# Performance work log

Measured on AMD Instinct MI355X. Metric: run time of the kernel, lower is better.

## Reference

```python
import jax, jax.numpy as jnp
import numpy as np

D = 1024   # model dim (hard-coded in ClsNet)
H = 16     # num_heads
HD = D // H
FF = 2048  # torch TransformerEncoderLayer default dim_feedforward
B, LX, LY = 8, 512, 512
EPS = 1e-5
NEG = -1e9


def setup_inputs() -> dict:
    key = jax.random.key(0)
    ks = jax.random.split(key, 16)
    s = 0.02
    inp = {
        "x": jax.random.normal(ks[0], (B, LX, D), jnp.float32),
        "y": jax.random.normal(ks[1], (B, LY, D), jnp.float32),
        "cls": jax.random.normal(ks[2], (D,), jnp.float32) * s,
        "sep": jax.random.normal(ks[3], (D,), jnp.float32) * s,
        "px": jax.random.normal(ks[4], (D,), jnp.float32) * s,
        "py": jax.random.normal(ks[5], (D,), jnp.float32) * s,
        "Wqkv": jax.random.normal(ks[6], (3 * D, D), jnp.float32) * s,
        "bqkv": jnp.zeros((3 * D,), jnp.float32),
        "Wo": jax.random.normal(ks[7], (D, D), jnp.float32) * s,
        "bo": jnp.zeros((D,), jnp.float32),
        "W1": jax.random.normal(ks[8], (FF, D), jnp.float32) * s,
        "b1": jnp.zeros((FF,), jnp.float32),
        "W2": jax.random.normal(ks[9], (D, FF), jnp.float32) * s,
        "b2": jnp.zeros((D,), jnp.float32),
        "ln1_g": jnp.ones((D,), jnp.float32),
        "ln1_b": jnp.zeros((D,), jnp.float32),
        "ln2_g": jnp.ones((D,), jnp.float32),
        "ln2_b": jnp.zeros((D,), jnp.float32),
        "x_len": jax.random.randint(ks[10], (B,), 1, LX + 1, jnp.int32),
        "y_len": jax.random.randint(ks[11], (B,), 1, LY + 1, jnp.int32),
    }
    return inp


def _merge(x, y, cls, sep, px, py, x_len, y_len):
    # Vectorized version of ClsNet.merge: [CLS] x_i+px ... [SEP] y_i+py ... [SEP] pad...
    Bn, Lx, Dd = x.shape
    Ly = y.shape[1]
    S = Lx + Ly + 3
    pos = jnp.arange(S)[None, :]            # [1,S]
    lx = x_len[:, None]                     # [B,1]
    ly = y_len[:, None]
    is_cls = pos == 0                       # [1,S]
    is_x = (pos >= 1) & (pos <= lx)         # [B,S]
    is_sep1 = pos == lx + 1
    is_y = (pos >= lx + 2) & (pos <= lx + ly + 1)
    is_sep2 = pos == lx + ly + 2
    xi = jnp.clip(pos - 1, 0, Lx - 1)       # [1,S]
    yi = jnp.clip(pos - lx - 2, 0, Ly - 1)  # [B,S]
    xg = jnp.take_along_axis(x, xi[:, :, None], axis=1)  # [B,S,D] (broadcast batch)
    yg = jnp.take_along_axis(y, yi[:, :, None], axis=1)  # [B,S,D]
    seq = (jnp.where(is_x[..., None], xg + px, 0.0)
           + jnp.where(is_y[..., None], yg + py, 0.0)
           + is_cls[..., None] * cls
           + (is_sep1 | is_sep2)[..., None] * sep)       # [B,S,D]
    mask = is_cls | is_x | is_sep1 | is_y | is_sep2      # [B,S] True = valid token
    return seq, mask


def _ln(h, g, b):
    m = jnp.mean(h, axis=-1, keepdims=True)
    v = jnp.mean(jnp.square(h - m), axis=-1, keepdims=True)
    return (h - m) * jax.lax.rsqrt(v + EPS) * g + b


def _encoder_layer(seq, mask, Wqkv, bqkv, Wo, bo, W1, b1, W2, b2, ln1_g, ln1_b, ln2_g, ln2_b):
    Bn, S, Dd = seq.shape
    qkv = seq @ Wqkv.T + bqkv                              # [B,S,3D]
    q, k, v = jnp.split(qkv, 3, axis=-1)
    q = q.reshape(Bn, S, H, HD)
    k = k.reshape(Bn, S, H, HD)
    v = v.reshape(Bn, S, H, HD)
    bias = jnp.where(mask, 0.0, NEG)[:, None, None, :]     # padded KEYS masked out
    scores = jnp.einsum("bqhd,bkhd->bhqk", q, k) / np.sqrt(HD) + bias
    attn = jax.nn.softmax(scores, axis=-1)
    o = jnp.einsum("bhqk,bkhd->bqhd", attn, v).reshape(Bn, S, Dd)
    o = o @ Wo.T + bo
    h = _ln(seq + o, ln1_g, ln1_b)                          # post-norm (torch default)
    f = jax.nn.relu(h @ W1.T + b1) @ W2.T + b2
    return _ln(h + f, ln2_g, ln2_b)


def reference(x, y, cls, sep, px, py, Wqkv, bqkv, Wo, bo, W1, b1, W2, b2,
              ln1_g, ln1_b, ln2_g, ln2_b, x_len, y_len):
    seq, mask = _merge(x, y, cls, sep, px, py, x_len, y_len)
    out = _encoder_layer(seq, mask, Wqkv, bqkv, Wo, bo, W1, b1, W2, b2,
                         ln1_g, ln1_b, ln2_g, ln2_b)
    # torch code returns a[0] of the seq-first tensor -> the CLS position for all batches
    return out[:, 0, :]
```

## Files before the change

kernel.cpp:

```cpp
#include <hip/hip_runtime.h>
#include <hip/hip_bf16.h>

#define D_ 1024
#define H_ 16
#define FF_ 2048
#define B_ 8
#define S_ 1027
#define MPAD_ 8320
#define PSTR_ 1056
#define EPS_ 1e-5f

typedef __hip_bfloat16 bf16;
typedef unsigned short u16;
typedef unsigned int u32;
typedef __attribute__((ext_vector_type(4))) float floatx4;
typedef __bf16 bf16x8 __attribute__((ext_vector_type(8)));

__device__ __forceinline__ float2 bfpair(u32 u) {
  union { u32 u; float f; } lo, hi;
  lo.u = u << 16; hi.u = u & 0xffff0000u;
  return make_float2(lo.f, hi.f);
}

__device__ __forceinline__ u32 f2bfbits(float f) {
  union { bf16 h; u16 u; } cv; cv.h = __float2bfloat16(f); return (u32)cv.u;
}

__device__ __forceinline__ float block_sum(float x, float* red) {
  const int t = threadIdx.x;
  __syncthreads();
  red[t] = x;
  __syncthreads();
  for (int s = 128; s > 0; s >>= 1) {
    if (t < s) red[t] += red[t + s];
    __syncthreads();
  }
  return red[0];
}

__device__ __forceinline__ float block_max(float x, float* red) {
  const int t = threadIdx.x;
  __syncthreads();
  red[t] = x;
  __syncthreads();
  for (int s = 128; s > 0; s >>= 1) {
    if (t < s) red[t] = fmaxf(red[t], red[t + s]);
    __syncthreads();
  }
  return red[0];
}

__global__ void __launch_bounds__(256) build_seq_kernel(
    const float* __restrict__ x, const float* __restrict__ y,
    const float* __restrict__ cls, const float* __restrict__ sep,
    const float* __restrict__ px, const float* __restrict__ py,
    const int* __restrict__ x_len, const int* __restrict__ y_len,
    bf16* __restrict__ seq) {
  const int m = blockIdx.x, t = threadIdx.x;
  const int b = m / S_;
  const int s = m - b * S_;
  if (b >= B_) return;
  const float* src = nullptr;
  const float* add = nullptr;
  const int lx = x_len[b], ly = y_len[b];
  if (s == 0) src = cls;
  else if (s <= lx) { src = x + ((size_t)b * 512 + (s - 1)) * D_; add = px; }
  else if (s == lx + 1) src = sep;
  else if (s <= lx + ly + 1) { src = y + ((size_t)b * 512 + (s - lx - 2)) * D_; add = py; }
  else if (s == lx + ly + 2) src = sep;
  if (!src) return;
  float4 sv = ((const float4*)src)[t];
  if (add) {
    float4 av = ((const float4*)add)[t];
    sv.x += av.x; sv.y += av.y; sv.z += av.z; sv.w += av.w;
  }
  uint2 o;
  o.x = f2bfbits(sv.x) | (f2bfbits(sv.y) << 16);
  o.y = f2bfbits(sv.z) | (f2bfbits(sv.w) << 16);
  ((uint2*)(seq + (size_t)m * D_))[t] = o;
}

__global__ void __launch_bounds__(256) qr_kernel(
    const float* __restrict__ cls, const float* __restrict__ Wqkv,
    const float* __restrict__ bqkv, u16* __restrict__ RT_hi,
    u16* __restrict__ RT_lo) {
  const int cc = blockIdx.x, h = blockIdx.y, t = threadIdx.x;
  __shared__ float clds[D_];
  __shared__ float qs[64];
  *(float4*)&clds[t * 4] = ((const float4*)cls)[t];
  __syncthreads();
  const int w = t >> 6, l = t & 63;
#pragma unroll 2
  for (int e8 = 0; e8 < 16; ++e8) {
    const int e = e8 * 4 + w;
    const float4* wr = (const float4*)(Wqkv + (size_t)(h * 64 + e) * D_) + l;
    float acc = 0.f;
#pragma unroll
    for (int c = 0; c < 4; ++c) {
      float4 wv = wr[c * 64];
      const float* cp = &clds[c * 256 + l * 4];
      acc += wv.x * cp[0] + wv.y * cp[1] + wv.z * cp[2] + wv.w * cp[3];
    }
#pragma unroll
    for (int off = 32; off > 0; off >>= 1) acc += __shfl_down(acc, off, 64);
    if (l == 0) qs[e] = (acc + bqkv[h * 64 + e]) * 0.125f;
  }
  __syncthreads();
  const int c = cc * 256 + t;
  const float* Wk = Wqkv + (size_t)(D_ + h * 64) * D_ + c;
  float acc = 0.f;
#pragma unroll 8
  for (int e = 0; e < 64; ++e) acc += Wk[(size_t)e * D_] * qs[e];
  const u32 hb = f2bfbits(acc);
  union { u32 u; float f; } hv; hv.u = hb << 16;
  RT_hi[h * D_ + c] = (u16)hb;
  RT_lo[h * D_ + c] = (u16)f2bfbits(acc - hv.f);
}

__global__ void __launch_bounds__(256) scores_kernel(
    const bf16* __restrict__ seq, const u16* __restrict__ RT_hi,
    const u16* __restrict__ RT_lo, const int* __restrict__ x_len,
    const int* __restrict__ y_len, float* __restrict__ S) {
  const int m0 = blockIdx.x * 64;
  bool valid = false;
#pragma unroll
  for (int b = 0; b < B_; ++b) {
    int rs = b * S_, re = rs + x_len[b] + y_len[b] + 3;
    if (m0 < re && m0 + 64 > rs) valid = true;
  }
  if (!valid) return;
  const int t = threadIdx.x;
  const int w = t >> 6, lane = t & 63, lane16 = lane & 15, quad = lane >> 4;
  const int row = m0 + w * 16 + lane16;
  const u16* arow = (const u16*)seq + (size_t)row * D_ + quad * 8;
  const u16* bh = RT_hi + lane16 * D_ + quad * 8;
  const u16* bl = RT_lo + lane16 * D_ + quad * 8;
  floatx4 acc = {};
#pragma unroll
  for (int kt = 0; kt < 32; ++kt) {
    bf16x8 a  = *(const bf16x8*)(arow + kt * 32);
    bf16x8 vh = *(const bf16x8*)(bh + kt * 32);
    bf16x8 vl = *(const bf16x8*)(bl + kt * 32);
    acc = __builtin_amdgcn_mfma_f32_16x16x32_bf16(a, vh, acc, 0, 0, 0);
    acc = __builtin_amdgcn_mfma_f32_16x16x32_bf16(a, vl, acc, 0, 0, 0);
  }
  *(floatx4*)&S[(size_t)lane16 * MPAD_ + m0 + w * 16 + quad * 4] = acc;
}

__global__ void __launch_bounds__(256) softmax_kernel(
    const float* __restrict__ S, const int* __restrict__ x_len,
    const int* __restrict__ y_len, u16* __restrict__ P) {
  const int h = blockIdx.x, b = blockIdx.y, t = threadIdx.x;
  const int n = x_len[b] + y_len[b] + 3;
  __shared__ float sc[PSTR_];
  __shared__ float red[256];
  const float* Sp = S + (size_t)h * MPAD_ + b * S_;
  float lmax = -3.0e38f;
  for (int k = t; k < n; k += 256) {
    float s = Sp[k];
    sc[k] = s;
    lmax = fmaxf(lmax, s);
  }
  const float gmax = block_max(lmax, red);
  float lsum = 0.f;
  for (int k = t; k < n; k += 256) {
    float p = __expf(sc[k] - gmax);
    sc[k] = p;
    lsum += p;
  }
  const float inv = 1.0f / block_sum(lsum, red);
  u16* Pp = P + (size_t)(h * 8 + b) * PSTR_;
  for (int k = t; k < PSTR_; k += 256)
    Pp[k] = (k < n) ? (u16)f2bfbits(sc[k] * inv) : (u16)0;
}

__global__ void __launch_bounds__(256) cbar_kernel(
    const bf16* __restrict__ seq, const u16* __restrict__ P,
    const int* __restrict__ x_len, const int* __restrict__ y_len,
    float* __restrict__ cbar) {
  const int ct = blockIdx.x, b = blockIdx.y, t = threadIdx.x;
  const int c0 = ct * 64;
  const int n = x_len[b] + y_len[b] + 3;
  const int nkt = (n + 31) >> 5;
  __shared__ u16 tile[32 * 68];
  const int w = t >> 6, lane = t & 63, lane16 = lane & 15, quad = lane >> 4;
  const int sk = t >> 3, scg = (t & 7) * 8;
  floatx4 acc = {};
  for (int kt = 0; kt < nkt; ++kt) {
    const int k0 = kt * 32;
    __syncthreads();
    uint4 v = make_uint4(0u, 0u, 0u, 0u);
    if (k0 + sk < n)
      v = *(const uint4*)((const u16*)seq + (size_t)(b * S_ + k0 + sk) * D_ + c0 + scg);
    *(uint2*)&tile[sk * 68 + scg]     = make_uint2(v.x, v.y);
    *(uint2*)&tile[sk * 68 + scg + 4] = make_uint2(v.z, v.w);
    __syncthreads();
    bf16x8 a = *(const bf16x8*)(P + (size_t)(lane16 * 8 + b) * PSTR_ + k0 + quad * 8);
    union { bf16x8 v; u16 u[8]; } bu;
#pragma unroll
    for (int j = 0; j < 8; ++j)
      bu.u[j] = tile[(quad * 8 + j) * 68 + w * 16 + lane16];
    acc = __builtin_amdgcn_mfma_f32_16x16x32_bf16(a, bu.v, acc, 0, 0, 0);
  }
#pragma unroll
  for (int r = 0; r < 4; ++r)
    cbar[(size_t)(b * 16 + quad * 4 + r) * D_ + c0 + w * 16 + lane16] = acc[r];
}

template <int K, int N, int BSTR, bool INBF, bool OUTBF, bool RELU, bool PERHEAD>
__global__ void __launch_bounds__(256) gemv8_kernel(
    const void* __restrict__ in_, const float* __restrict__ W,
    const float* __restrict__ bias, void* __restrict__ out_) {
  const int t = threadIdx.x;
  const int hoff = PERHEAD ? ((blockIdx.x * 4) >> 6) * D_ : 0;
  __shared__ u16 lsb[INBF ? 8 * K : 1];
  __shared__ float lsf[INBF ? 1 : 8 * K];
  if (INBF) {
    const u16* in = (const u16*)in_;
    const int per = 8 * K / (256 * 8);
#pragma unroll
    for (int i = 0; i < per; ++i) {
      int flat = (t + i * 256) * 8;
      int b = flat / K, k = flat % K;
      *(uint4*)&lsb[flat] = *(const uint4*)(in + (size_t)b * BSTR + hoff + k);
    }
  } else {
    const float* in = (const float*)in_;
    const int per = 8 * K / (256 * 4);
#pragma unroll
    for (int i = 0; i < per; ++i) {
      int flat = (t + i * 256) * 4;
      int b = flat / K, k = flat % K;
      *(float4*)&lsf[flat] = *(const float4*)(in + (size_t)b * BSTR + hoff + k);
    }
  }
  __syncthreads();
  const int w = t >> 6, l = t & 63;
  const int r = blockIdx.x * 4 + w;
  float acc[8] = {};
#pragma unroll
  for (int ch = 0; ch < K / 256; ++ch) {
    float4 wv = *(const float4*)(W + (size_t)r * K + ch * 256 + l * 4);
#pragma unroll
    for (int b = 0; b < 8; ++b) {
      float i0, i1, i2, i3;
      if (INBF) {
        uint2 u = *(const uint2*)&lsb[b * K + ch * 256 + l * 4];
        float2 p0 = bfpair(u.x), p1 = bfpair(u.y);
        i0 = p0.x; i1 = p0.y; i2 = p1.x; i3 = p1.y;
      } else {
        const float* p = &lsf[b * K + ch * 256 + l * 4];
        i0 = p[0]; i1 = p[1]; i2 = p[2]; i3 = p[3];
      }
      acc[b] += wv.x * i0 + wv.y * i1 + wv.z * i2 + wv.w * i3;
    }
  }
#pragma unroll
  for (int off = 32; off > 0; off >>= 1)
#pragma unroll
    for (int b = 0; b < 8; ++b) acc[b] += __shfl_down(acc[b], off, 64);
  if (l == 0) {
    const float bs = bias[r];
#pragma unroll
    for (int b = 0; b < 8; ++b) {
      float v = acc[b] + bs;
      if (RELU) v = fmaxf(v, 0.f);
      if (OUTBF) ((bf16*)out_)[(size_t)b * N + r] = __float2bfloat16(v);
      else       ((float*)out_)[(size_t)b * N + r] = v;
    }
  }
}

__global__ void __launch_bounds__(256) w1ln_kernel(
    const float* __restrict__ att, const float* __restrict__ cls,
    const float* __restrict__ g1, const float* __restrict__ be1,
    const float* __restrict__ W1, const float* __restrict__ b1,
    bf16* __restrict__ f1) {
  const int t = threadIdx.x;
  __shared__ float ls[8 * D_];
  __shared__ float mn[8], rsd[8];
  float4 cv = ((const float4*)cls)[t];
#pragma unroll
  for (int i = 0; i < 8; ++i) {
    float4 a = ((const float4*)(att + (size_t)i * D_))[t];
    a.x += cv.x; a.y += cv.y; a.z += cv.z; a.w += cv.w;
    *(float4*)&ls[i * D_ + t * 4] = a;
  }
  __syncthreads();
  {
    const int b = t >> 5, j = t & 31;
    const float* base = &ls[b * D_ + j * 32];
    float s = 0.f, s2 = 0.f;
#pragma unroll
    for (int k = 0; k < 32; ++k) { float v = base[k]; s += v; s2 += v * v; }
#pragma unroll
    for (int off = 16; off > 0; off >>= 1) {
      s += __shfl_down(s, off, 32);
      s2 += __shfl_down(s2, off, 32);
    }
    if (j == 0) {
      float mean = s * (1.f / D_);
      mn[b] = mean;
      rsd[b] = rsqrtf(s2 * (1.f / D_) - mean * mean + EPS_);
    }
  }
  __syncthreads();
  {
    const int b = t >> 5, j = t & 31;
    const float mean = mn[b], rs = rsd[b];
    float* base = &ls[b * D_ + j * 32];
    const float* gp = &g1[j * 32];
    const float* bp = &be1[j * 32];
#pragma unroll
    for (int k = 0; k < 32; ++k)
      base[k] = (base[k] - mean) * rs * gp[k] + bp[k];
  }
  __syncthreads();
  const int w = t >> 6, l = t & 63;
  const int r = blockIdx.x * 4 + w;
  float acc[8] = {};
#pragma unroll
  for (int ch = 0; ch < 4; ++ch) {
    float4 wv = *(const float4*)(W1 + (size_t)r * D_ + ch * 256 + l * 4);
#pragma unroll
    for (int b = 0; b < 8; ++b) {
      const float* p = &ls[b * D_ + ch * 256 + l * 4];
      acc[b] += wv.x * p[0] + wv.y * p[1] + wv.z * p[2] + wv.w * p[3];
    }
  }
#pragma unroll
  for (int off = 32; off > 0; off >>= 1)
#pragma unroll
    for (int b = 0; b < 8; ++b) acc[b] += __shfl_down(acc[b], off, 64);
  if (l == 0) {
    const float bs = b1[r];
#pragma unroll
    for (int b = 0; b < 8; ++b)
      f1[(size_t)b * FF_ + r] = __float2bfloat16(fmaxf(acc[b] + bs, 0.f));
  }
}

__global__ void __launch_bounds__(256) ln2_kernel(
    const float* __restrict__ cls, const float* __restrict__ att,
    const float* __restrict__ f2, const float* __restrict__ g1,
    const float* __restrict__ be1, const float* __restrict__ g2,
    const float* __restrict__ be2, float* __restrict__ out) {
  const int b = blockIdx.x, t = threadIdx.x;
  __shared__ float v[D_];
  __shared__ float red[256];
  for (int i = t; i < D_; i += 256) v[i] = cls[i] + att[(size_t)b * D_ + i];
  __syncthreads();
  float ls = 0.f;
  for (int i = t; i < D_; i += 256) ls += v[i];
  const float m1 = block_sum(ls, red) * (1.f / D_);
  float lv = 0.f;
  for (int i = t; i < D_; i += 256) { float dk = v[i] - m1; lv += dk * dk; }
  const float rs1 = rsqrtf(block_sum(lv, red) * (1.f / D_) + EPS_);
  __syncthreads();
  for (int i = t; i < D_; i += 256)
    v[i] = (v[i] - m1) * rs1 * g1[i] + be1[i] + f2[(size_t)b * D_ + i];
  __syncthreads();
  float ls2 = 0.f;
  for (int i = t; i < D_; i += 256) ls2 += v[i];
  const float m2 = block_sum(ls2, red) * (1.f / D_);
  float lv2 = 0.f;
  for (int i = t; i < D_; i += 256) { float dk = v[i] - m2; lv2 += dk * dk; }
  const float rs2 = rsqrtf(block_sum(lv2, red) * (1.f / D_) + EPS_);
  for (int i = t; i < D_; i += 256)
    out[(size_t)b * D_ + i] = (v[i] - m2) * rs2 * g2[i] + be2[i];
}

extern "C" void kernel_launch(void* const* d_in, const int* in_sizes, int n_in,
                              void* d_out, int out_size, void* d_ws, size_t ws_size,
                              hipStream_t stream) {
  (void)in_sizes; (void)n_in; (void)out_size; (void)ws_size;
  const float* x    = (const float*)d_in[0];
  const float* y    = (const float*)d_in[1];
  const float* cls  = (const float*)d_in[2];
  const float* sep  = (const float*)d_in[3];
  const float* px   = (const float*)d_in[4];
  const float* py   = (const float*)d_in[5];
  const float* Wqkv = (const float*)d_in[6];
  const float* bqkv = (const float*)d_in[7];
  const float* Wo   = (const float*)d_in[8];
  const float* bo   = (const float*)d_in[9];
  const float* W1   = (const float*)d_in[10];
  const float* b1   = (const float*)d_in[11];
  const float* W2   = (const float*)d_in[12];
  const float* b2   = (const float*)d_in[13];
  const float* g1   = (const float*)d_in[14];
  const float* be1  = (const float*)d_in[15];
  const float* g2   = (const float*)d_in[16];
  const float* be2  = (const float*)d_in[17];
  const int* xl     = (const int*)d_in[18];
  const int* yl     = (const int*)d_in[19];

  char* ws = (char*)d_ws;
  bf16*  seq   = (bf16*)(ws);
  u16*   RT_hi = (u16*)(ws + 17039360);
  u16*   RT_lo = (u16*)(ws + 17072128);
  float* S     = (float*)(ws + 17104896);
  u16*   P     = (u16*)(ws + 17637376);
  float* cbar  = (float*)(ws + 17907712);
  float* o0    = (float*)(ws + 18432000);
  float* att   = (float*)(ws + 18464768);
  bf16*  f1    = (bf16*)(ws + 18497536);
  float* f2    = (float*)(ws + 18530304);

  build_seq_kernel<<<MPAD_, 256, 0, stream>>>(x, y, cls, sep, px, py, xl, yl, seq);
  qr_kernel<<<dim3(4, 16), 256, 0, stream>>>(cls, Wqkv, bqkv, RT_hi, RT_lo);
  scores_kernel<<<130, 256, 0, stream>>>(seq, RT_hi, RT_lo, xl, yl, S);
  softmax_kernel<<<dim3(16, 8), 256, 0, stream>>>(S, xl, yl, P);
  cbar_kernel<<<dim3(16, 8), 256, 0, stream>>>(seq, P, xl, yl, cbar);
  gemv8_kernel<1024, 1024, 16384, false, false, false, true>
      <<<256, 256, 0, stream>>>(cbar, Wqkv + (size_t)2048 * 1024, bqkv + 2048, o0);
  gemv8_kernel<1024, 1024, 1024, false, false, false, false>
      <<<256, 256, 0, stream>>>(o0, Wo, bo, att);
  w1ln_kernel<<<512, 256, 0, stream>>>(att, cls, g1, be1, W1, b1, f1);
  gemv8_kernel<2048, 1024, 2048, true, false, false, false>
      <<<256, 256, 0, stream>>>(f1, W2, b2, f2);
  ln2_kernel<<<B_, 256, 0, stream>>>(cls, att, f2, g1, be1, g2, be2,
                                     (float*)d_out);
}
```

Before: 205.9 us.

## Fuse all encoder stages into one cooperative persistent kernel with grid syncs

```diff
diff --git a/kernel.cpp b/kernel.cpp
--- a/kernel.cpp
+++ b/kernel.cpp
@@ -1,5 +1,8 @@
 #include <hip/hip_runtime.h>
 #include <hip/hip_bf16.h>
+#include <hip/hip_cooperative_groups.h>
+
+namespace cg = cooperative_groups;
 
 #define D_ 1024
 #define H_ 16
@@ -48,6 +51,359 @@
     __syncthreads();
   }
   return red[0];
+}
+
+struct SMemD { float sc[PSTR_]; float red[256]; };
+struct SMemJ { float v[D_]; float red[256]; };
+union SMemU {
+  float qs_[64];
+  SMemD d;
+  u16 tile[32 * 68];
+  float lsf[8 * D_];
+  u16 lsb[8 * FF_];
+  SMemJ j;
+};
+struct SMem { SMemU u; float mn[8]; float rsd[8]; };
+
+__global__ void __launch_bounds__(256) fused_kernel2(
+    const float* __restrict__ x, const float* __restrict__ y,
+    const float* __restrict__ cls, const float* __restrict__ sep,
+    const float* __restrict__ px, const float* __restrict__ py,
+    const float* __restrict__ Wqkv, const float* __restrict__ bqkv,
+    const float* __restrict__ Wo, const float* __restrict__ bo,
+    const float* __restrict__ W1, const float* __restrict__ b1,
+    const float* __restrict__ W2, const float* __restrict__ b2,
+    const float* __restrict__ g1, const float* __restrict__ be1,
+    const float* __restrict__ g2, const float* __restrict__ be2,
+    const int* __restrict__ xl, const int* __restrict__ yl,
+    bf16* __restrict__ seq, float* __restrict__ q0s,
+    u16* __restrict__ RT_hi, u16* __restrict__ RT_lo,
+    float* __restrict__ S, u16* __restrict__ P, float* __restrict__ cbar,
+    float* __restrict__ o0, float* __restrict__ att, bf16* __restrict__ f1,
+    float* __restrict__ f2, float* __restrict__ outv) {
+  cg::grid_group grid = cg::this_grid();
+  const int bid = blockIdx.x, t = threadIdx.x;
+  const int w = t >> 6, l = t & 63;
+  const int lane16 = l & 15, quad = l >> 4;
+  __shared__ SMem sm;
+
+  {
+    const int r = bid * 4 + w;
+    const float4* wr = (const float4*)(Wqkv + (size_t)r * D_) + l;
+    const float4* cl4 = (const float4*)cls + l;
+    float acc = 0.f;
+#pragma unroll
+    for (int c = 0; c < 4; ++c) {
+      float4 wv = wr[c * 64], cv = cl4[c * 64];
+      acc += wv.x * cv.x + wv.y * cv.y + wv.z * cv.z + wv.w * cv.w;
+    }
+#pragma unroll
+    for (int off = 32; off > 0; off >>= 1) acc += __shfl_down(acc, off, 64);
+    if (l == 0) q0s[r] = (acc + bqkv[r]) * 0.125f;
+  }
+  for (int m = bid; m < B_ * S_; m += 256) {
+    const int b = m / S_;
+    const int s = m - b * S_;
+    const float* src = nullptr;
+    const float* add = nullptr;
+    const int lx = xl[b], ly = yl[b];
+    if (s == 0) src = cls;
+    else if (s <= lx) { src = x + ((size_t)b * 512 + (s - 1)) * D_; add = px; }
+    else if (s == lx + 1) src = sep;
+    else if (s <= lx + ly + 1) { src = y + ((size_t)b * 512 + (s - lx - 2)) * D_; add = py; }
+    else if (s == lx + ly + 2) src = sep;
+    if (!src) continue;
+    float4 sv = ((const float4*)src)[t];
+    if (add) {
+      float4 av = ((const float4*)add)[t];
+      sv.x += av.x; sv.y += av.y; sv.z += av.z; sv.w += av.w;
+    }
+    uint2 o;
+    o.x = f2bfbits(sv.x) | (f2bfbits(sv.y) << 16);
+    o.y = f2bfbits(sv.z) | (f2bfbits(sv.w) << 16);
+    ((uint2*)(seq + (size_t)m * D_))[t] = o;
+  }
+  grid.sync();
+
+  if (bid < 64) {
+    const int h = bid >> 2, cc = bid & 3;
+    if (t < 64) sm.u.qs_[t] = q0s[h * 64 + t];
+    __syncthreads();
+    const int c = cc * 256 + t;
+    const float* Wk = Wqkv + (size_t)(D_ + h * 64) * D_ + c;
+    float acc = 0.f;
+#pragma unroll 8
+    for (int e = 0; e < 64; ++e) acc += Wk[(size_t)e * D_] * sm.u.qs_[e];
+    const u32 hb = f2bfbits(acc);
+    union { u32 u; float f; } hv; hv.u = hb << 16;
+    RT_hi[h * D_ + c] = (u16)hb;
+    RT_lo[h * D_ + c] = (u16)f2bfbits(acc - hv.f);
+  }
+  grid.sync();
+
+  if (bid < 130) {
+    const int m0 = bid * 64;
+    bool valid = false;
+#pragma unroll
+    for (int b = 0; b < B_; ++b) {
+      int rs = b * S_, re = rs + xl[b] + yl[b] + 3;
+      if (m0 < re && m0 + 64 > rs) valid = true;
+    }
+    if (valid) {
+      const int row = m0 + w * 16 + lane16;
+      const u16* arow = (const u16*)seq + (size_t)row * D_ + quad * 8;
+      const u16* bh = RT_hi + lane16 * D_ + quad * 8;
+      const u16* bl = RT_lo + lane16 * D_ + quad * 8;
+      floatx4 acc = {};
+#pragma unroll 4
+      for (int kt = 0; kt < 32; ++kt) {
+        bf16x8 a  = *(const bf16x8*)(arow + kt * 32);
+        bf16x8 vh = *(const bf16x8*)(bh + kt * 32);
+        bf16x8 vl = *(const bf16x8*)(bl + kt * 32);
+        acc = __builtin_amdgcn_mfma_f32_16x16x32_bf16(a, vh, acc, 0, 0, 0);
+        acc = __builtin_amdgcn_mfma_f32_16x16x32_bf16(a, vl, acc, 0, 0, 0);
+      }
+      *(floatx4*)&S[(size_t)lane16 * MPAD_ + m0 + w * 16 + quad * 4] = acc;
+    }
+  }
+  grid.sync();
+
+  if (bid < 128) {
+    const int h = bid >> 3, b = bid & 7;
+    const int n = xl[b] + yl[b] + 3;
+    const float* Sp = S + (size_t)h * MPAD_ + b * S_;
+    float lmax = -3.0e38f;
+    for (int k = t; k < n; k += 256) {
+      float s = Sp[k];
+      sm.u.d.sc[k] = s;
+      lmax = fmaxf(lmax, s);
+    }
+    const float gmax = block_max(lmax, sm.u.d.red);
+    float lsum = 0.f;
+    for (int k = t; k < n; k += 256) {
+      float p = __expf(sm.u.d.sc[k] - gmax);
+      sm.u.d.sc[k] = p;
+      lsum += p;
+    }
+    const float inv = 1.0f / block_sum(lsum, sm.u.d.red);
+    u16* Pp = P + (size_t)(h * 8 + b) * PSTR_;
+    for (int k = t; k < PSTR_; k += 256)
+      Pp[k] = (k < n) ? (u16)f2bfbits(sm.u.d.sc[k] * inv) : (u16)0;
+  }
+  grid.sync();
+
+  if (bid < 128) {
+    const int ct = bid >> 3, b = bid & 7;
+    const int c0 = ct * 64;
+    const int n = xl[b] + yl[b] + 3;
+    const int nkt = (n + 31) >> 5;
+    const int sk = t >> 3, scg = (t & 7) * 8;
+    const u16* Pp = P + (size_t)(lane16 * 8 + b) * PSTR_;
+    floatx4 acc = {};
+    for (int kt = 0; kt < nkt; ++kt) {
+      const int k0 = kt * 32;
+      __syncthreads();
+      uint4 v = make_uint4(0u, 0u, 0u, 0u);
+      if (k0 + sk < n)
+        v = *(const uint4*)((const u16*)seq + (size_t)(b * S_ + k0 + sk) * D_ + c0 + scg);
+      *(uint2*)&sm.u.tile[sk * 68 + scg]     = make_uint2(v.x, v.y);
+      *(uint2*)&sm.u.tile[sk * 68 + scg + 4] = make_uint2(v.z, v.w);
+      __syncthreads();
+      bf16x8 a = *(const bf16x8*)(Pp + k0 + quad * 8);
+      union { bf16x8 v; u16 u[8]; } bu;
+#pragma unroll
+      for (int j = 0; j < 8; ++j)
+        bu.u[j] = sm.u.tile[(quad * 8 + j) * 68 + w * 16 + lane16];
+      acc = __builtin_amdgcn_mfma_f32_16x16x32_bf16(a, bu.v, acc, 0, 0, 0);
+    }
+#pragma unroll
+    for (int r = 0; r < 4; ++r)
+      cbar[(size_t)(b * 16 + quad * 4 + r) * D_ + c0 + w * 16 + lane16] = acc[r];
+  }
+  grid.sync();
+
+  {
+    const int hoff = (bid >> 4) * D_;
+#pragma unroll
+    for (int i = 0; i < 8; ++i) {
+      int flat = (t + i * 256) * 4;
+      int b = flat >> 10, k = flat & 1023;
+      *(float4*)&sm.u.lsf[flat] = *(const float4*)(cbar + (size_t)b * 16384 + hoff + k);
+    }
+    __syncthreads();
+    const int r = bid * 4 + w;
+    const float* Wv = Wqkv + (size_t)2048 * D_;
+    float acc[8] = {};
+#pragma unroll
+    for (int ch = 0; ch < 4; ++ch) {
+      float4 wv = *(const float4*)(Wv + (size_t)r * D_ + ch * 256 + l * 4);
+#pragma unroll
+      for (int b = 0; b < 8; ++b) {
+        const float* p = &sm.u.lsf[b * D_ + ch * 256 + l * 4];
+        acc[b] += wv.x * p[0] + wv.y * p[1] + wv.z * p[2] + wv.w * p[3];
+      }
+    }
+#pragma unroll
+    for (int off = 32; off > 0; off >>= 1)
+#pragma unroll
+      for (int b = 0; b < 8; ++b) acc[b] += __shfl_down(acc[b], off, 64);
+    if (l == 0) {
+      const float bs = bqkv[2048 + r];
+#pragma unroll
+      for (int b = 0; b < 8; ++b) o0[(size_t)b * D_ + r] = acc[b] + bs;
+    }
+  }
+  grid.sync();
+
+  {
+#pragma unroll
+    for (int i = 0; i < 8; ++i) {
+      int flat = (t + i * 256) * 4;
+      *(float4*)&sm.u.lsf[flat] = *(const float4*)(o0 + flat);
+    }
+    __syncthreads();
+    const int r = bid * 4 + w;
+    float acc[8] = {};
+#pragma unroll
+    for (int ch = 0; ch < 4; ++ch) {
+      float4 wv = *(const float4*)(Wo + (size_t)r * D_ + ch * 256 + l * 4);
+#pragma unroll
+      for (int b = 0; b < 8; ++b) {
+        const float* p = &sm.u.lsf[b * D_ + ch * 256 + l * 4];
+        acc[b] += wv.x * p[0] + wv.y * p[1] + wv.z * p[2] + wv.w * p[3];
+      }
+    }
+#pragma unroll
+    for (int off = 32; off > 0; off >>= 1)
+#pragma unroll
+      for (int b = 0; b < 8; ++b) acc[b] += __shfl_down(acc[b], off, 64);
+    if (l == 0) {
+      const float bs = bo[r];
+#pragma unroll
+      for (int b = 0; b < 8; ++b) att[(size_t)b * D_ + r] = acc[b] + bs;
+    }
+  }
+  grid.sync();
+
+  {
+    float4 cv = ((const float4*)cls)[t];
+#pragma unroll
+    for (int i = 0; i < 8; ++i) {
+      float4 a = ((const float4*)(att + (size_t)i * D_))[t];
+      a.x += cv.x; a.y += cv.y; a.z += cv.z; a.w += cv.w;
+      *(float4*)&sm.u.lsf[i * D_ + t * 4] = a;
+    }
+    __syncthreads();
+    {
+      const int b = t >> 5, j = t & 31;
+      const float* base = &sm.u.lsf[b * D_ + j * 32];
+      float s = 0.f, s2 = 0.f;
+#pragma unroll
+      for (int k = 0; k < 32; ++k) { float v = base[k]; s += v; s2 += v * v; }
+#pragma unroll
+      for (int off = 16; off > 0; off >>= 1) {
+        s += __shfl_down(s, off, 32);
+        s2 += __shfl_down(s2, off, 32);
+      }
+      if (j == 0) {
+        float mean = s * (1.f / D_);
+        sm.mn[b] = mean;
+        sm.rsd[b] = rsqrtf(s2 * (1.f / D_) - mean * mean + EPS_);
+      }
+    }
+    __syncthreads();
+    {
+      const int b = t >> 5, j = t & 31;
+      const float mean = sm.mn[b], rs = sm.rsd[b];
+      float* base = &sm.u.lsf[b * D_ + j * 32];
+      const float* gp = &g1[j * 32];
+      const float* bp = &be1[j * 32];
+#pragma unroll
+      for (int k = 0; k < 32; ++k)
+        base[k] = (base[k] - mean) * rs * gp[k] + bp[k];
+    }
+    __syncthreads();
+#pragma unroll
+    for (int rr = 0; rr < 2; ++rr) {
+      const int r = bid * 8 + rr * 4 + w;
+      float acc[8] = {};
+#pragma unroll
+      for (int ch = 0; ch < 4; ++ch) {
+        float4 wv = *(const float4*)(W1 + (size_t)r * D_ + ch * 256 + l * 4);
+#pragma unroll
+        for (int b = 0; b < 8; ++b) {
+          const float* p = &sm.u.lsf[b * D_ + ch * 256 + l * 4];
+          acc[b] += wv.x * p[0] + wv.y * p[1] + wv.z * p[2] + wv.w * p[3];
+        }
+      }
+#pragma unroll
+      for (int off = 32; off > 0; off >>= 1)
+#pragma unroll
+        for (int b = 0; b < 8; ++b) acc[b] += __shfl_down(acc[b], off, 64);
+      if (l == 0) {
+        const float bs = b1[r];
+#pragma unroll
+        for (int b = 0; b < 8; ++b)
+          f1[(size_t)b * FF_ + r] = __float2bfloat16(fmaxf(acc[b] + bs, 0.f));
+      }
+    }
+  }
+  grid.sync();
+
+  {
+#pragma unroll
+    for (int i = 0; i < 8; ++i) {
+      int flat = (t + i * 256) * 8;
+      *(uint4*)&sm.u.lsb[flat] = *(const uint4*)((const u16*)f1 + flat);
+    }
+    __syncthreads();
+    const int r = bid * 4 + w;
+    float acc[8] = {};
+#pragma unroll
+    for (int ch = 0; ch < 8; ++ch) {
+      float4 wv = *(const float4*)(W2 + (size_t)r * FF_ + ch * 256 + l * 4);
+#pragma unroll
+      for (int b = 0; b < 8; ++b) {
+        uint2 u = *(const uint2*)&sm.u.lsb[b * FF_ + ch * 256 + l * 4];
+        float2 p0 = bfpair(u.x), p1 = bfpair(u.y);
+        acc[b] += wv.x * p0.x + wv.y * p0.y + wv.z * p1.x + wv.w * p1.y;
+      }
+    }
+#pragma unroll
+    for (int off = 32; off > 0; off >>= 1)
+#pragma unroll
+      for (int b = 0; b < 8; ++b) acc[b] += __shfl_down(acc[b], off, 64);
+    if (l == 0) {
+      const float bs = b2[r];
+#pragma unroll
+      for (int b = 0; b < 8; ++b) f2[(size_t)b * D_ + r] = acc[b] + bs;
+    }
+  }
+  grid.sync();
+
+  if (bid < 8) {
+    const int b = bid;
+    for (int i = t; i < D_; i += 256) sm.u.j.v[i] = cls[i] + att[(size_t)b * D_ + i];
+    __syncthreads();
+    float ls = 0.f;
+    for (int i = t; i < D_; i += 256) ls += sm.u.j.v[i];
+    const float m1 = block_sum(ls, sm.u.j.red) * (1.f / D_);
+    float lv = 0.f;
+    for (int i = t; i < D_; i += 256) { float dk = sm.u.j.v[i] - m1; lv += dk * dk; }
+    const float rs1 = rsqrtf(block_sum(lv, sm.u.j.red) * (1.f / D_) + EPS_);
+    __syncthreads();
+    for (int i = t; i < D_; i += 256)
+      sm.u.j.v[i] = (sm.u.j.v[i] - m1) * rs1 * g1[i] + be1[i] + f2[(size_t)b * D_ + i];
+    __syncthreads();
+    float ls2 = 0.f;
+    for (int i = t; i < D_; i += 256) ls2 += sm.u.j.v[i];
+    const float m2 = block_sum(ls2, sm.u.j.red) * (1.f / D_);
+    float lv2 = 0.f;
+    for (int i = t; i < D_; i += 256) { float dk = sm.u.j.v[i] - m2; lv2 += dk * dk; }
+    const float rs2 = rsqrtf(block_sum(lv2, sm.u.j.red) * (1.f / D_) + EPS_);
+    for (int i = t; i < D_; i += 256)
+      outv[(size_t)b * D_ + i] = (sm.u.j.v[i] - m2) * rs2 * g2[i] + be2[i];
+  }
 }
 
 __global__ void __launch_bounds__(256) build_seq_kernel(
@@ -136,7 +492,7 @@
   const u16* bh = RT_hi + lane16 * D_ + quad * 8;
   const u16* bl = RT_lo + lane16 * D_ + quad * 8;
   floatx4 acc = {};
-#pragma unroll
+#pragma unroll 4
   for (int kt = 0; kt < 32; ++kt) {
     bf16x8 a  = *(const bf16x8*)(arow + kt * 32);
     bf16x8 vh = *(const bf16x8*)(bh + kt * 32);
@@ -397,28 +753,41 @@
 
   char* ws = (char*)d_ws;
   bf16*  seq   = (bf16*)(ws);
-  u16*   RT_hi = (u16*)(ws + 17039360);
-  u16*   RT_lo = (u16*)(ws + 17072128);
-  float* S     = (float*)(ws + 17104896);
-  u16*   P     = (u16*)(ws + 17637376);
-  float* cbar  = (float*)(ws + 17907712);
-  float* o0    = (float*)(ws + 18432000);
-  float* att   = (float*)(ws + 18464768);
-  bf16*  f1    = (bf16*)(ws + 18497536);
-  float* f2    = (float*)(ws + 18530304);
-
-  build_seq_kernel<<<MPAD_, 256, 0, stream>>>(x, y, cls, sep, px, py, xl, yl, seq);
-  qr_kernel<<<dim3(4, 16), 256, 0, stream>>>(cls, Wqkv, bqkv, RT_hi, RT_lo);
-  scores_kernel<<<130, 256, 0, stream>>>(seq, RT_hi, RT_lo, xl, yl, S);
-  softmax_kernel<<<dim3(16, 8), 256, 0, stream>>>(S, xl, yl, P);
-  cbar_kernel<<<dim3(16, 8), 256, 0, stream>>>(seq, P, xl, yl, cbar);
-  gemv8_kernel<1024, 1024, 16384, false, false, false, true>
-      <<<256, 256, 0, stream>>>(cbar, Wqkv + (size_t)2048 * 1024, bqkv + 2048, o0);
-  gemv8_kernel<1024, 1024, 1024, false, false, false, false>
-      <<<256, 256, 0, stream>>>(o0, Wo, bo, att);
-  w1ln_kernel<<<512, 256, 0, stream>>>(att, cls, g1, be1, W1, b1, f1);
-  gemv8_kernel<2048, 1024, 2048, true, false, false, false>
-      <<<256, 256, 0, stream>>>(f1, W2, b2, f2);
-  ln2_kernel<<<B_, 256, 0, stream>>>(cls, att, f2, g1, be1, g2, be2,
-                                     (float*)d_out);
-}
+  float* q0s   = (float*)(ws + 17039360);
+  u16*   RT_hi = (u16*)(ws + 17043456);
+  u16*   RT_lo = (u16*)(ws + 17076224);
+  float* S     = (float*)(ws + 17108992);
+  u16*   P     = (u16*)(ws + 17641472);
+  float* cbar  = (float*)(ws + 17911808);
+  float* o0    = (float*)(ws + 18436096);
+  float* att   = (float*)(ws + 18468864);
+  bf16*  f1    = (bf16*)(ws + 18501632);
+  float* f2    = (float*)(ws + 18534400);
+  float* outv  = (float*)d_out;
+
+  void* args[] = {
+    (void*)&x, (void*)&y, (void*)&cls, (void*)&sep, (void*)&px, (void*)&py,
+    (void*)&Wqkv, (void*)&bqkv, (void*)&Wo, (void*)&bo, (void*)&W1, (void*)&b1,
+    (void*)&W2, (void*)&b2, (void*)&g1, (void*)&be1, (void*)&g2, (void*)&be2,
+    (void*)&xl, (void*)&yl, (void*)&seq, (void*)&q0s, (void*)&RT_hi,
+    (void*)&RT_lo, (void*)&S, (void*)&P, (void*)&cbar, (void*)&o0, (void*)&att,
+    (void*)&f1, (void*)&f2, (void*)&outv
+  };
+  hipError_t err = hipLaunchCooperativeKernel(
+      (const void*)fused_kernel2, dim3(256), dim3(256), args, 0, stream);
+  if (err != hipSuccess) {
+    build_seq_kernel<<<MPAD_, 256, 0, stream>>>(x, y, cls, sep, px, py, xl, yl, seq);
+    qr_kernel<<<dim3(4, 16), 256, 0, stream>>>(cls, Wqkv, bqkv, RT_hi, RT_lo);
+    scores_kernel<<<130, 256, 0, stream>>>(seq, RT_hi, RT_lo, xl, yl, S);
+    softmax_kernel<<<dim3(16, 8), 256, 0, stream>>>(S, xl, yl, P);
+    cbar_kernel<<<dim3(16, 8), 256, 0, stream>>>(seq, P, xl, yl, cbar);
+    gemv8_kernel<1024, 1024, 16384, false, false, false, true>
+        <<<256, 256, 0, stream>>>(cbar, Wqkv + (size_t)2048 * 1024, bqkv + 2048, o0);
+    gemv8_kernel<1024, 1024, 1024, false, false, false, false>
+        <<<256, 256, 0, stream>>>(o0, Wo, bo, att);
+    w1ln_kernel<<<512, 256, 0, stream>>>(att, cls, g1, be1, W1, b1, f1);
+    gemv8_kernel<2048, 1024, 2048, true, false, false, false>
+        <<<256, 256, 0, stream>>>(f1, W2, b2, f2);
+    ln2_kernel<<<B_, 256, 0, stream>>>(cls, att, f2, g1, be1, g2, be2, outv);
+  }
+}
```

Result: slower. 480.0 us (+133.1%).

## Fuse seq build with query projection and softmax into cbar kernel

Applied to the files above, without the earlier changes.

```diff
diff --git a/kernel.cpp b/kernel.cpp
--- a/kernel.cpp
+++ b/kernel.cpp
@@ -7,7 +7,7 @@
 #define B_ 8
 #define S_ 1027
 #define MPAD_ 8320
-#define PSTR_ 1056
+#define PLSTR_ 1060
 #define EPS_ 1e-5f
 
 typedef __hip_bfloat16 bf16;
@@ -38,53 +38,41 @@
   return red[0];
 }
 
-__device__ __forceinline__ float block_max(float x, float* red) {
-  const int t = threadIdx.x;
-  __syncthreads();
-  red[t] = x;
-  __syncthreads();
-  for (int s = 128; s > 0; s >>= 1) {
-    if (t < s) red[t] = fmaxf(red[t], red[t + s]);
-    __syncthreads();
-  }
-  return red[0];
-}
-
-__global__ void __launch_bounds__(256) build_seq_kernel(
+__global__ void __launch_bounds__(256) seq_qr_kernel(
     const float* __restrict__ x, const float* __restrict__ y,
     const float* __restrict__ cls, const float* __restrict__ sep,
     const float* __restrict__ px, const float* __restrict__ py,
+    const float* __restrict__ Wqkv, const float* __restrict__ bqkv,
     const int* __restrict__ x_len, const int* __restrict__ y_len,
-    bf16* __restrict__ seq) {
-  const int m = blockIdx.x, t = threadIdx.x;
-  const int b = m / S_;
-  const int s = m - b * S_;
-  if (b >= B_) return;
-  const float* src = nullptr;
-  const float* add = nullptr;
-  const int lx = x_len[b], ly = y_len[b];
-  if (s == 0) src = cls;
-  else if (s <= lx) { src = x + ((size_t)b * 512 + (s - 1)) * D_; add = px; }
-  else if (s == lx + 1) src = sep;
-  else if (s <= lx + ly + 1) { src = y + ((size_t)b * 512 + (s - lx - 2)) * D_; add = py; }
-  else if (s == lx + ly + 2) src = sep;
-  if (!src) return;
-  float4 sv = ((const float4*)src)[t];
-  if (add) {
-    float4 av = ((const float4*)add)[t];
-    sv.x += av.x; sv.y += av.y; sv.z += av.z; sv.w += av.w;
-  }
-  uint2 o;
-  o.x = f2bfbits(sv.x) | (f2bfbits(sv.y) << 16);
-  o.y = f2bfbits(sv.z) | (f2bfbits(sv.w) << 16);
-  ((uint2*)(seq + (size_t)m * D_))[t] = o;
-}
-
-__global__ void __launch_bounds__(256) qr_kernel(
-    const float* __restrict__ cls, const float* __restrict__ Wqkv,
-    const float* __restrict__ bqkv, u16* __restrict__ RT_hi,
-    u16* __restrict__ RT_lo) {
-  const int cc = blockIdx.x, h = blockIdx.y, t = threadIdx.x;
+    bf16* __restrict__ seq, u16* __restrict__ RT_hi, u16* __restrict__ RT_lo) {
+  const int t = threadIdx.x;
+  if (blockIdx.x < MPAD_) {
+    const int m = blockIdx.x;
+    const int b = m / S_;
+    const int s = m - b * S_;
+    if (b >= B_) return;
+    const float* src = nullptr;
+    const float* add = nullptr;
+    const int lx = x_len[b], ly = y_len[b];
+    if (s == 0) src = cls;
+    else if (s <= lx) { src = x + ((size_t)b * 512 + (s - 1)) * D_; add = px; }
+    else if (s == lx + 1) src = sep;
+    else if (s <= lx + ly + 1) { src = y + ((size_t)b * 512 + (s - lx - 2)) * D_; add = py; }
+    else if (s == lx + ly + 2) src = sep;
+    if (!src) return;
+    float4 sv = ((const float4*)src)[t];
+    if (add) {
+      float4 av = ((const float4*)add)[t];
+      sv.x += av.x; sv.y += av.y; sv.z += av.z; sv.w += av.w;
+    }
+    uint2 o;
+    o.x = f2bfbits(sv.x) | (f2bfbits(sv.y) << 16);
+    o.y = f2bfbits(sv.z) | (f2bfbits(sv.w) << 16);
+    ((uint2*)(seq + (size_t)m * D_))[t] = o;
+    return;
+  }
+  const int bid2 = blockIdx.x - MPAD_;
+  const int cc = bid2 & 3, h = bid2 >> 2;
   __shared__ float clds[D_];
   __shared__ float qs[64];
   *(float4*)&clds[t * 4] = ((const float4*)cls)[t];
@@ -136,7 +124,7 @@
   const u16* bh = RT_hi + lane16 * D_ + quad * 8;
   const u16* bl = RT_lo + lane16 * D_ + quad * 8;
   floatx4 acc = {};
-#pragma unroll
+#pragma unroll 4
   for (int kt = 0; kt < 32; ++kt) {
     bf16x8 a  = *(const bf16x8*)(arow + kt * 32);
     bf16x8 vh = *(const bf16x8*)(bh + kt * 32);
@@ -147,43 +135,42 @@
   *(floatx4*)&S[(size_t)lane16 * MPAD_ + m0 + w * 16 + quad * 4] = acc;
 }
 
-__global__ void __launch_bounds__(256) softmax_kernel(
-    const float* __restrict__ S, const int* __restrict__ x_len,
-    const int* __restrict__ y_len, u16* __restrict__ P) {
-  const int h = blockIdx.x, b = blockIdx.y, t = threadIdx.x;
-  const int n = x_len[b] + y_len[b] + 3;
-  __shared__ float sc[PSTR_];
-  __shared__ float red[256];
-  const float* Sp = S + (size_t)h * MPAD_ + b * S_;
-  float lmax = -3.0e38f;
-  for (int k = t; k < n; k += 256) {
-    float s = Sp[k];
-    sc[k] = s;
-    lmax = fmaxf(lmax, s);
-  }
-  const float gmax = block_max(lmax, red);
-  float lsum = 0.f;
-  for (int k = t; k < n; k += 256) {
-    float p = __expf(sc[k] - gmax);
-    sc[k] = p;
-    lsum += p;
-  }
-  const float inv = 1.0f / block_sum(lsum, red);
-  u16* Pp = P + (size_t)(h * 8 + b) * PSTR_;
-  for (int k = t; k < PSTR_; k += 256)
-    Pp[k] = (k < n) ? (u16)f2bfbits(sc[k] * inv) : (u16)0;
-}
-
-__global__ void __launch_bounds__(256) cbar_kernel(
-    const bf16* __restrict__ seq, const u16* __restrict__ P,
+__global__ void __launch_bounds__(256) cbar_sm_kernel(
+    const float* __restrict__ S, const bf16* __restrict__ seq,
     const int* __restrict__ x_len, const int* __restrict__ y_len,
     float* __restrict__ cbar) {
   const int ct = blockIdx.x, b = blockIdx.y, t = threadIdx.x;
   const int c0 = ct * 64;
   const int n = x_len[b] + y_len[b] + 3;
   const int nkt = (n + 31) >> 5;
+  const int w = t >> 6, l = t & 63;
+  const int lane16 = l & 15, quad = l >> 4;
+  __shared__ u16 pls[16 * PLSTR_];
+  __shared__ float inv16[16];
   __shared__ u16 tile[32 * 68];
-  const int w = t >> 6, lane = t & 63, lane16 = lane & 15, quad = lane >> 4;
+#pragma unroll
+  for (int j = 0; j < 4; ++j) {
+    const int h = w * 4 + j;
+    const float* Sp = S + (size_t)h * MPAD_ + b * S_;
+    float lmax = -3.0e38f;
+    for (int k = l; k < n; k += 64) lmax = fmaxf(lmax, Sp[k]);
+#pragma unroll
+    for (int off = 32; off > 0; off >>= 1)
+      lmax = fmaxf(lmax, __shfl_xor(lmax, off, 64));
+    float lsum = 0.f;
+    for (int k = l; k < n; k += 64) {
+      float p = __expf(Sp[k] - lmax);
+      u32 pb = f2bfbits(p);
+      pls[h * PLSTR_ + k] = (u16)pb;
+      union { u32 u; float f; } pf; pf.u = pb << 16;
+      lsum += pf.f;
+    }
+    for (int k = n + l; k < nkt * 32; k += 64) pls[h * PLSTR_ + k] = 0;
+#pragma unroll
+    for (int off = 32; off > 0; off >>= 1) lsum += __shfl_xor(lsum, off, 64);
+    if (l == 0) inv16[h] = 1.0f / lsum;
+  }
+  __syncthreads();
   const int sk = t >> 3, scg = (t & 7) * 8;
   floatx4 acc = {};
   for (int kt = 0; kt < nkt; ++kt) {
@@ -195,7 +182,7 @@
     *(uint2*)&tile[sk * 68 + scg]     = make_uint2(v.x, v.y);
     *(uint2*)&tile[sk * 68 + scg + 4] = make_uint2(v.z, v.w);
     __syncthreads();
-    bf16x8 a = *(const bf16x8*)(P + (size_t)(lane16 * 8 + b) * PSTR_ + k0 + quad * 8);
+    bf16x8 a = *(const bf16x8*)&pls[lane16 * PLSTR_ + k0 + quad * 8];
     union { bf16x8 v; u16 u[8]; } bu;
 #pragma unroll
     for (int j = 0; j < 8; ++j)
@@ -204,7 +191,8 @@
   }
 #pragma unroll
   for (int r = 0; r < 4; ++r)
-    cbar[(size_t)(b * 16 + quad * 4 + r) * D_ + c0 + w * 16 + lane16] = acc[r];
+    cbar[(size_t)(b * 16 + quad * 4 + r) * D_ + c0 + w * 16 + lane16] =
+        acc[r] * inv16[quad * 4 + r];
 }
 
 template <int K, int N, int BSTR, bool INBF, bool OUTBF, bool RELU, bool PERHEAD>
@@ -400,18 +388,17 @@
   u16*   RT_hi = (u16*)(ws + 17039360);
   u16*   RT_lo = (u16*)(ws + 17072128);
   float* S     = (float*)(ws + 17104896);
-  u16*   P     = (u16*)(ws + 17637376);
-  float* cbar  = (float*)(ws + 17907712);
-  float* o0    = (float*)(ws + 18432000);
-  float* att   = (float*)(ws + 18464768);
-  bf16*  f1    = (bf16*)(ws + 18497536);
-  float* f2    = (float*)(ws + 18530304);
-
-  build_seq_kernel<<<MPAD_, 256, 0, stream>>>(x, y, cls, sep, px, py, xl, yl, seq);
-  qr_kernel<<<dim3(4, 16), 256, 0, stream>>>(cls, Wqkv, bqkv, RT_hi, RT_lo);
+  float* cbar  = (float*)(ws + 17637376);
+  float* o0    = (float*)(ws + 18161664);
+  float* att   = (float*)(ws + 18194432);
+  bf16*  f1    = (bf16*)(ws + 18227200);
+  float* f2    = (float*)(ws + 18259968);
+
+  seq_qr_kernel<<<MPAD_ + 64, 256, 0, stream>>>(x, y, cls, sep, px, py,
+                                                Wqkv, bqkv, xl, yl,
+                                                seq, RT_hi, RT_lo);
   scores_kernel<<<130, 256, 0, stream>>>(seq, RT_hi, RT_lo, xl, yl, S);
-  softmax_kernel<<<dim3(16, 8), 256, 0, stream>>>(S, xl, yl, P);
-  cbar_kernel<<<dim3(16, 8), 256, 0, stream>>>(seq, P, xl, yl, cbar);
+  cbar_sm_kernel<<<dim3(16, 8), 256, 0, stream>>>(S, seq, xl, yl, cbar);
   gemv8_kernel<1024, 1024, 16384, false, false, false, true>
       <<<256, 256, 0, stream>>>(cbar, Wqkv + (size_t)2048 * 1024, bqkv + 2048, o0);
   gemv8_kernel<1024, 1024, 1024, false, false, false, false>
```

New measurement: 211.8 us. 1.03x slower.
